# Optimization experiments

Measured on AMD Instinct MI355X. Metric: run time of the kernel, lower is better.

Reference implementation:

```python
import jax, jax.numpy as jnp
import numpy as np

# ---- single-qubit gate matrices (theta may be scalar or batched (N,)) ----

def _rx(theta):
    t = theta * 0.5
    c = jnp.cos(t).astype(jnp.complex64)
    s = jnp.sin(t).astype(jnp.complex64)
    return jnp.stack([jnp.stack([c, -1j * s], -1), jnp.stack([-1j * s, c], -1)], -2)

def _ry(theta):
    t = theta * 0.5
    c = jnp.cos(t).astype(jnp.complex64)
    s = jnp.sin(t).astype(jnp.complex64)
    return jnp.stack([jnp.stack([c, -s], -1), jnp.stack([s, c], -1)], -2)

def _rz(theta):
    t = theta * 0.5
    e = jnp.exp(-1j * t.astype(jnp.complex64))
    z = jnp.zeros_like(e)
    return jnp.stack([jnp.stack([e, z], -1), jnp.stack([z, jnp.conj(e)], -1)], -2)

def _apply_1q(state, U, wire):
    # state: (N, 2^P) complex; U: (2,2) shared or (N,2,2) per-sample
    N = state.shape[0]
    s = state.reshape(N, 2 ** wire, 2, -1)
    if U.ndim == 3:
        s = jnp.einsum('nab,nxby->nxay', U, s)
    else:
        s = jnp.einsum('ab,nxby->nxay', U, s)
    return s.reshape(N, -1)

def _apply_cnot(state, c, t, P):
    # flip target axis where control bit == 1
    N = state.shape[0]
    s = state.reshape((N,) + (2,) * P)
    ac, at = 1 + c, 1 + t
    s0 = jnp.take(s, 0, axis=ac)
    s1 = jnp.take(s, 1, axis=ac)
    at2 = at if at < ac else at - 1
    s1 = jnp.flip(s1, axis=at2)
    s = jnp.stack([s0, s1], axis=ac)
    return s.reshape(N, -1)

def _circuit(angles, qweights, P):
    # angles: (N, P, 3); qweights: (L, P, 3) -> expvals (N, P)
    N = angles.shape[0]
    state = jnp.zeros((N, 2 ** P), jnp.complex64).at[:, 0].set(1.0)
    for i in range(P):  # encoding rotations (per-sample)
        state = _apply_1q(state, _rx(angles[:, i, 0]), i)
        state = _apply_1q(state, _ry(angles[:, i, 1]), i)
        state = _apply_1q(state, _rz(angles[:, i, 2]), i)
    for L in range(qweights.shape[0]):  # variational layers (shared weights)
        for i in range(P):
            state = _apply_1q(state, _ry(qweights[L, i, 0]), i)
            state = _apply_1q(state, _rz(qweights[L, i, 1]), i)
            state = _apply_1q(state, _ry(qweights[L, i, 2]), i)
        for i in range(P):  # ring CNOTs
            state = _apply_cnot(state, i, (i + 1) % P, P)
    probs = jnp.real(state * jnp.conj(state))  # (N, 2^P)
    idx = jnp.arange(2 ** P)
    bits = (idx[None, :] >> (P - 1 - jnp.arange(P))[:, None]) & 1  # wire 0 = MSB
    signs = (1 - 2 * bits).astype(jnp.float32)  # (P, 2^P)
    return probs @ signs.T  # <Z_i> per wire, (N, P)

def setup_inputs() -> dict:
    key = jax.random.key(0)
    ks = jax.random.split(key, 6)
    B, T, P, D, L = 2, 128, 13, 64, 2
    h = jax.random.normal(ks[0], (B, T, P, D), jnp.float32)
    enc_w = jax.random.normal(ks[1], (3, D), jnp.float32) * (1.0 / np.sqrt(D))
    enc_b = jax.random.normal(ks[2], (3,), jnp.float32) * 0.1
    qweights = jax.random.normal(ks[3], (L, P, 3), jnp.float32)
    dec_w = jax.random.normal(ks[4], (D, 1), jnp.float32) * 0.1
    alpha = jnp.full((1,), 0.05, jnp.float32)
    return {"h": h, "enc_w": enc_w, "enc_b": enc_b, "qweights": qweights, "dec_w": dec_w, "alpha": alpha}

def reference(h, enc_w, enc_b, qweights, dec_w, alpha):
    B, T, P, D = h.shape
    # encoder: Linear(D, 3)
    angles = (jnp.einsum('btpd,ad->btpa', h, enc_w) + enc_b).reshape(B * T, P, 3)
    expvals = _circuit(angles, qweights, P)  # (B*T, P)
    # decoder: Linear(1, D, bias=False)
    decoded = (expvals[:, :, None] * dec_w[:, 0][None, None, :]).reshape(B, T, P, D)
    return h + alpha[0] * decoded
```

## Files before the change

kernel.cpp:

```cpp
#include <hip/hip_runtime.h>

#define P   13
#define BLK 512
#define NH  (P * 64)

typedef float2 c2;

__device__ __forceinline__ c2 cmul2(c2 a, c2 b) {
    return make_float2(a.x * b.x - a.y * b.y, a.x * b.y + a.y * b.x);
}
__device__ __forceinline__ c2 cfma2(c2 a, c2 b, c2 c) {
    return make_float2(fmaf(a.x, b.x, fmaf(-a.y, b.y, c.x)),
                       fmaf(a.x, b.y, fmaf( a.y, b.x, c.y)));
}
__device__ __forceinline__ c2 shflx2(c2 v, int m) {
    c2 r;
    r.x = __shfl_xor(v.x, m, 64);
    r.y = __shfl_xor(v.y, m, 64);
    return r;
}


__global__ __launch_bounds__(BLK) void qlc_kernel(
    const float* __restrict__ h, const float* __restrict__ enc_w,
    const float* __restrict__ enc_b, const float* __restrict__ qw,
    const float* __restrict__ dec_w, const float* __restrict__ alpha,
    float* __restrict__ out, int nlayers)
{
    const int n    = blockIdx.x;
    const int tid  = threadIdx.x;
    const int lane = tid & 63;
    const int wv   = tid >> 6;

    __shared__ float lds[16384];
    float* re = lds;
    float* im = lds + 8192;

    c2 s[16];

    for (int p = wv; p < P; p += 8) {
        float hv = h[(size_t)n * NH + p * 64 + lane];
        float a0 = hv * enc_w[lane];
        float a1 = hv * enc_w[64 + lane];
        float a2 = hv * enc_w[128 + lane];
#pragma unroll
        for (int m = 32; m; m >>= 1) {
            a0 += __shfl_xor(a0, m, 64);
            a1 += __shfl_xor(a1, m, 64);
            a2 += __shfl_xor(a2, m, 64);
        }
        float x = 0.5f * (a0 + enc_b[0]);
        float y = 0.5f * (a1 + enc_b[1]);
        float z = 0.5f * (a2 + enc_b[2]);
        float cx = cosf(x), sx = sinf(x);
        float cy = cosf(y), sy = sinf(y);
        float cz = cosf(z), sz = sinf(z);
        c2 em = {cz, -sz}, ep = {cz, sz};
        c2 u0 = cmul2(em, make_float2(cy * cx,  sy * sx));
        c2 u1 = cmul2(ep, make_float2(sy * cx, -cy * sx));
        c2 w0 = u0, w1 = u1;
        if (nlayers > 0) {
            const float* w = qw + p * 3;
            float a = 0.5f * w[0], b = 0.5f * w[1], c = 0.5f * w[2];
            float ca = cosf(a), sa = sinf(a);
            float cb = cosf(b), sb = sinf(b);
            float cc = cosf(c), sc = sinf(c);
            c2 B00 = { ca * cb, -ca * sb};
            c2 B01 = {-sa * cb,  sa * sb};
            c2 B10 = { sa * cb,  sa * sb};
            c2 B11 = { ca * cb,  ca * sb};
            c2 V00 = {cc * B00.x - sc * B10.x, cc * B00.y - sc * B10.y};
            c2 V01 = {cc * B01.x - sc * B11.x, cc * B01.y - sc * B11.y};
            c2 V10 = {sc * B00.x + cc * B10.x, sc * B00.y + cc * B10.y};
            c2 V11 = {sc * B01.x + cc * B11.x, sc * B01.y + cc * B11.y};
            w0 = cfma2(V00, u0, cmul2(V01, u1));
            w1 = cfma2(V10, u0, cmul2(V11, u1));
        }
        if (lane == 0) {
            lds[p * 4 + 0] = w0.x; lds[p * 4 + 1] = w0.y;
            lds[p * 4 + 2] = w1.x; lds[p * 4 + 3] = w1.y;
        }
    }
    __syncthreads();
    {
        c2 pref = {1.f, 0.f};
#pragma unroll
        for (int w = 0; w < 9; ++w) {
            int b = (tid >> (8 - w)) & 1;
            c2 vp = {lds[w * 4 + b * 2], lds[w * 4 + b * 2 + 1]};
            pref = cmul2(pref, vp);
        }
        c2 w9[2], w10[2], w11[2], w12[2];
#pragma unroll
        for (int b = 0; b < 2; ++b) {
            w9[b]  = {lds[ 9 * 4 + b * 2], lds[ 9 * 4 + b * 2 + 1]};
            w10[b] = {lds[10 * 4 + b * 2], lds[10 * 4 + b * 2 + 1]};
            w11[b] = {lds[11 * 4 + b * 2], lds[11 * 4 + b * 2 + 1]};
            w12[b] = {lds[12 * 4 + b * 2], lds[12 * 4 + b * 2 + 1]};
        }
#pragma unroll
        for (int r = 0; r < 16; ++r)
            s[r] = cmul2(pref, cmul2(cmul2(w9[(r >> 3) & 1], w10[(r >> 2) & 1]),
                                     cmul2(w11[(r >> 1) & 1], w12[r & 1])));
    }

    auto cnot_chain = [&]() {
        __syncthreads();
        {
            int c = (tid >> 8) & 1;
            if (c) {
#pragma unroll
                for (int r = 0; r < 16; ++r) { re[r * 512 + tid] = s[r].x; im[r * 512 + tid] = s[r].y; }
            }
            __syncthreads();
            if (c) {
                int p = tid ^ 128;
#pragma unroll
                for (int r = 0; r < 16; ++r) s[r] = make_float2(re[r * 512 + p], im[r * 512 + p]);
            }
        }
        __syncthreads();
        {
            int c = (tid >> 7) & 1;
            if (c) {
#pragma unroll
                for (int r = 0; r < 16; ++r) { re[r * 512 + tid] = s[r].x; im[r * 512 + tid] = s[r].y; }
            }
            __syncthreads();
            if (c) {
                int p = tid ^ 64;
#pragma unroll
                for (int r = 0; r < 16; ++r) s[r] = make_float2(re[r * 512 + p], im[r * 512 + p]);
            }
        }
        {
            int c = (tid >> 6) & 1;
#pragma unroll
            for (int r = 0; r < 16; ++r) { c2 pv = shflx2(s[r], 32); if (c) s[r] = pv; }
        }
#pragma unroll
        for (int k = 0; k < 5; ++k) {
            int cb = 5 - k, m = 1 << (4 - k);
            int c = (lane >> cb) & 1;
#pragma unroll
            for (int r = 0; r < 16; ++r) { c2 pv = shflx2(s[r], m); if (c) s[r] = pv; }
        }
        {
            int c = lane & 1;
#pragma unroll
            for (int r = 0; r < 8; ++r) {
                c2 a = s[r], b = s[r + 8];
                s[r]     = c ? b : a;
                s[r + 8] = c ? a : b;
            }
        }
#pragma unroll
        for (int r = 0; r < 16; ++r)
            if ((r & 8) && !(r & 4)) { c2 t = s[r]; s[r] = s[r | 4]; s[r | 4] = t; }
#pragma unroll
        for (int r = 0; r < 16; ++r)
            if ((r & 4) && !(r & 2)) { c2 t = s[r]; s[r] = s[r | 2]; s[r | 2] = t; }
#pragma unroll
        for (int r = 0; r < 16; ++r)
            if ((r & 2) && !(r & 1)) { c2 t = s[r]; s[r] = s[r | 1]; s[r | 1] = t; }
        __syncthreads();
#pragma unroll
        for (int r = 1; r < 16; r += 2) { re[r * 512 + tid] = s[r].x; im[r * 512 + tid] = s[r].y; }
        __syncthreads();
        {
            int p = tid ^ 256;
#pragma unroll
            for (int r = 1; r < 16; r += 2) s[r] = make_float2(re[r * 512 + p], im[r * 512 + p]);
        }
    };

    auto apply_layer = [&](int l) {
        __syncthreads();
        if (tid < P) {
            const float* w = qw + (size_t)(l * P + tid) * 3;
            float a = 0.5f * w[0], b = 0.5f * w[1], c = 0.5f * w[2];
            float ca = cosf(a), sa = sinf(a);
            float cb = cosf(b), sb = sinf(b);
            float cc = cosf(c), sc = sinf(c);
            c2 B00 = { ca * cb, -ca * sb};
            c2 B01 = {-sa * cb,  sa * sb};
            c2 B10 = { sa * cb,  sa * sb};
            c2 B11 = { ca * cb,  ca * sb};
            float* m = lds + tid * 8;
            m[0] = cc * B00.x - sc * B10.x; m[1] = cc * B00.y - sc * B10.y;
            m[2] = cc * B01.x - sc * B11.x; m[3] = cc * B01.y - sc * B11.y;
            m[4] = sc * B00.x + cc * B10.x; m[5] = sc * B00.y + cc * B10.y;
            m[6] = sc * B01.x + cc * B11.x; m[7] = sc * B01.y + cc * B11.y;
        }
        __syncthreads();
#pragma unroll
        for (int p = 9; p <= 12; ++p) {
            int b = 12 - p;
            c2 u00 = {lds[p * 8 + 0], lds[p * 8 + 1]}, u01 = {lds[p * 8 + 2], lds[p * 8 + 3]};
            c2 u10 = {lds[p * 8 + 4], lds[p * 8 + 5]}, u11 = {lds[p * 8 + 6], lds[p * 8 + 7]};
#pragma unroll
            for (int r = 0; r < 16; ++r)
                if (!(r & (1 << b))) {
                    int r1 = r | (1 << b);
                    c2 a0 = s[r], a1 = s[r1];
                    s[r]  = cfma2(u00, a0, cmul2(u01, a1));
                    s[r1] = cfma2(u10, a0, cmul2(u11, a1));
                }
        }
#pragma unroll
        for (int p = 3; p <= 8; ++p) {
            int lb = 8 - p;
            c2 u00 = {lds[p * 8 + 0], lds[p * 8 + 1]}, u01 = {lds[p * 8 + 2], lds[p * 8 + 3]};
            c2 u10 = {lds[p * 8 + 4], lds[p * 8 + 5]}, u11 = {lds[p * 8 + 6], lds[p * 8 + 7]};
            int mb = (lane >> lb) & 1;
            c2 ua = mb ? u11 : u00;
            c2 ub = mb ? u10 : u01;
#pragma unroll
            for (int r = 0; r < 16; ++r) {
                c2 pv = shflx2(s[r], 1 << lb);
                s[r] = cfma2(ua, s[r], cmul2(ub, pv));
            }
        }
        c2 um[3][4];
#pragma unroll
        for (int p = 0; p < 3; ++p) {
            um[p][0] = {lds[p * 8 + 0], lds[p * 8 + 1]};
            um[p][1] = {lds[p * 8 + 2], lds[p * 8 + 3]};
            um[p][2] = {lds[p * 8 + 4], lds[p * 8 + 5]};
            um[p][3] = {lds[p * 8 + 6], lds[p * 8 + 7]};
        }
#pragma unroll
        for (int p = 0; p < 3; ++p) {
            int shift = 8 - p;
            __syncthreads();
#pragma unroll
            for (int r = 0; r < 16; ++r) { re[r * 512 + tid] = s[r].x; im[r * 512 + tid] = s[r].y; }
            __syncthreads();
            int pt = tid ^ (1 << shift);
            int mb = (tid >> shift) & 1;
            c2 ua = mb ? um[p][3] : um[p][0];
            c2 ub = mb ? um[p][2] : um[p][1];
#pragma unroll
            for (int r = 0; r < 16; ++r) {
                c2 pv = make_float2(re[r * 512 + pt], im[r * 512 + pt]);
                s[r] = cfma2(ua, s[r], cmul2(ub, pv));
            }
        }
    };

    if (nlayers > 0) cnot_chain();
    for (int l = 1; l < nlayers; ++l) { apply_layer(l); cnot_chain(); }

    float tot = 0.f, e9 = 0.f, e10 = 0.f, e11 = 0.f, e12 = 0.f;
#pragma unroll
    for (int r = 0; r < 16; ++r) {
        float pr = fmaf(s[r].x, s[r].x, s[r].y * s[r].y);
        tot += pr;
        e9  += (r & 8) ? -pr : pr;
        e10 += (r & 4) ? -pr : pr;
        e11 += (r & 2) ? -pr : pr;
        e12 += (r & 1) ? -pr : pr;
    }
    float v[13];
#pragma unroll
    for (int w = 0; w < 9; ++w) v[w] = ((tid >> (8 - w)) & 1) ? -tot : tot;
    v[9] = e9; v[10] = e10; v[11] = e11; v[12] = e12;
#pragma unroll
    for (int w = 0; w < 13; ++w) {
#pragma unroll
        for (int m = 32; m; m >>= 1) v[w] += __shfl_xor(v[w], m, 64);
    }
    __syncthreads();
    if (lane == 0) {
#pragma unroll
        for (int w = 0; w < 13; ++w) lds[wv * 13 + w] = v[w];
    }
    __syncthreads();
    if (tid < 13) {
        float sum = 0.f;
        for (int q = 0; q < 8; ++q) sum += lds[q * 13 + tid];
        lds[256 + tid] = sum;
    }
    __syncthreads();
    float al = alpha[0];
    for (int idx = tid; idx < NH; idx += BLK) {
        size_t off = (size_t)n * NH + idx;
        out[off] = fmaf(al * lds[256 + (idx >> 6)], dec_w[idx & 63], h[off]);
    }
}

extern "C" void kernel_launch(void* const* d_in, const int* in_sizes, int n_in,
                              void* d_out, int out_size, void* d_ws, size_t ws_size,
                              hipStream_t stream) {
    const float* h     = (const float*)d_in[0];
    const float* enc_w = (const float*)d_in[1];
    const float* enc_b = (const float*)d_in[2];
    const float* qw    = (const float*)d_in[3];
    const float* dec_w = (const float*)d_in[4];
    const float* alpha = (const float*)d_in[5];
    float* out = (float*)d_out;

    int N = in_sizes[0] / NH;
    int L = in_sizes[3] / (P * 3);

    qlc_kernel<<<N, BLK, 0, stream>>>(h, enc_w, enc_b, qw, dec_w, alpha, out, L);
}
```

Baseline: 91.11 us.

## Absorb CNOT rings into GF(2) basis-frame tracking instead of physically permuting state

Replaces the explicit CNOT-ring permutations (LDS round-trips and shuffles) with compile-time and runtime tracking of a linear GF(2) change of basis. The initial product state is built directly in the permuted frame, layer gates are applied along the transformed bit masks, and the Z expectations are read through parity masks. A specialised path for two layers uses constexpr masks so the gates map onto plain register, lane-shuffle and three LDS exchanges. It also switches to __sincosf and stores the state in LDS as interleaved float2. This removes several barrier-heavy shared-memory exchanges per layer, but the logic is intricate and __sincosf is less accurate than sinf/cosf.

```diff
diff --git a/kernel.cpp b/kernel.cpp
--- a/kernel.cpp
+++ b/kernel.cpp
@@ -14,12 +14,64 @@
                        fmaf(a.x, b.y, fmaf( a.y, b.x, c.y)));
 }
 __device__ __forceinline__ c2 shflx2(c2 v, int m) {
-    c2 r;
-    r.x = __shfl_xor(v.x, m, 64);
-    r.y = __shfl_xor(v.y, m, 64);
-    return r;
-}
-
+    c2 r; r.x = __shfl_xor(v.x, m, 64); r.y = __shfl_xor(v.y, m, 64); return r;
+}
+
+struct RowSet { unsigned r[13]; };
+constexpr RowSet chain_rows(RowSet f) {
+    for (int i = 0; i < 13; ++i) { int bc = 12 - i; int bt = (i == 12) ? 12 : (11 - i); f.r[bt] ^= f.r[bc]; }
+    return f;
+}
+constexpr RowSet chain_cols(RowSet g) {
+    for (int i = 0; i < 13; ++i) { int bc = 12 - i; int bt = (i == 12) ? 12 : (11 - i); g.r[bc] ^= g.r[bt]; }
+    return g;
+}
+constexpr RowSet R0c {{0x0C00,0x0801,0x0003,0x0006,0x000C,0x0018,0x0030,0x0060,0x00C0,0x0180,0x0300,0x1600,0x1400}};
+constexpr RowSet G0c {{0x1400,0x1C00,0x1C01,0x1C03,0x1C07,0x1C0F,0x1C1F,0x1C3F,0x1C7F,0x1CFF,0x1DFF,0x1FFF,0x0FFF}};
+constexpr RowSet F1c = chain_rows(R0c);
+constexpr RowSet F2c = chain_rows(F1c);
+constexpr RowSet G1c = chain_cols(G0c);
+static_assert(G1c.r[0]==0x0400 && G1c.r[1]==0x0800 && G1c.r[2]==0x0001 && G1c.r[3]==0x0002 &&
+              G1c.r[4]==0x0004 && G1c.r[5]==0x0008 && G1c.r[6]==0x0010 && G1c.r[7]==0x0020 &&
+              G1c.r[8]==0x0040 && G1c.r[9]==0x0080 && G1c.r[10]==0x0100 && G1c.r[11]==0x0200 &&
+              G1c.r[12]==0x1000, "single-bit gate masks after chain 1");
+static_assert(F1c.r[0]==0x0400 && F1c.r[1]==0x0800 && F1c.r[2]==0x0001 && F1c.r[12]==0x1000,
+              "frame after chain 1 is the bit-permutation phi");
+
+__device__ __forceinline__ void build_V(float wa, float wb, float wc, c2* u) {
+    float a = 0.5f * wa, b = 0.5f * wb, c = 0.5f * wc;
+    float sa, ca, sb, cb, sc, cc;
+    __sincosf(a, &sa, &ca); __sincosf(b, &sb, &cb); __sincosf(c, &sc, &cc);
+    float A = ca * cb, Bq = ca * sb, C = sa * cb, D = sa * sb;
+    u[0] = make_float2( cc * A - sc * C, -cc * Bq - sc * D);
+    u[1] = make_float2(-cc * C - sc * A,  cc * D - sc * Bq);
+    u[2] = make_float2( sc * A + cc * C, -sc * Bq + cc * D);
+    u[3] = make_float2(-sc * C + cc * A,  sc * D + cc * Bq);
+}
+
+template<int K>
+__device__ __forceinline__ void gate_reg(c2* s, const float* m) {
+    c2 u00 = {m[0], m[1]}, u01 = {m[2], m[3]}, u10 = {m[4], m[5]}, u11 = {m[6], m[7]};
+#pragma unroll
+    for (int r = 0; r < 16; ++r)
+        if (!(r & (1 << K))) {
+            const int r1 = r | (1 << K);
+            c2 a0 = s[r], a1 = s[r1];
+            s[r]  = cfma2(u00, a0, cmul2(u01, a1));
+            s[r1] = cfma2(u10, a0, cmul2(u11, a1));
+        }
+}
+template<int LM>
+__device__ __forceinline__ void gate_lane(c2* s, const float* m, int lane) {
+    c2 u00 = {m[0], m[1]}, u01 = {m[2], m[3]}, u10 = {m[4], m[5]}, u11 = {m[6], m[7]};
+    int mb = (lane & LM) ? 1 : 0;
+    c2 ua = mb ? u11 : u00, ub = mb ? u10 : u01;
+#pragma unroll
+    for (int r = 0; r < 16; ++r) {
+        c2 pv = shflx2(s[r], LM);
+        s[r] = cfma2(ua, s[r], cmul2(ub, pv));
+    }
+}
 
 __global__ __launch_bounds__(BLK) void qlc_kernel(
     const float* __restrict__ h, const float* __restrict__ enc_w,
@@ -27,265 +79,193 @@
     const float* __restrict__ dec_w, const float* __restrict__ alpha,
     float* __restrict__ out, int nlayers)
 {
-    const int n    = blockIdx.x;
-    const int tid  = threadIdx.x;
-    const int lane = tid & 63;
-    const int wv   = tid >> 6;
-
-    __shared__ float lds[16384];
-    float* re = lds;
-    float* im = lds + 8192;
-
+    const int n = blockIdx.x, tid = threadIdx.x, lane = tid & 63, wv = tid >> 6;
+    __shared__ c2 plane[8192];
+    float* smem = (float*)plane;
+    float* vec  = smem;
+    float* mats = smem + 64;
     c2 s[16];
 
     for (int p = wv; p < P; p += 8) {
         float hv = h[(size_t)n * NH + p * 64 + lane];
-        float a0 = hv * enc_w[lane];
-        float a1 = hv * enc_w[64 + lane];
-        float a2 = hv * enc_w[128 + lane];
+        float a0 = hv * enc_w[lane], a1 = hv * enc_w[64 + lane], a2 = hv * enc_w[128 + lane];
 #pragma unroll
         for (int m = 32; m; m >>= 1) {
-            a0 += __shfl_xor(a0, m, 64);
-            a1 += __shfl_xor(a1, m, 64);
-            a2 += __shfl_xor(a2, m, 64);
-        }
-        float x = 0.5f * (a0 + enc_b[0]);
-        float y = 0.5f * (a1 + enc_b[1]);
-        float z = 0.5f * (a2 + enc_b[2]);
-        float cx = cosf(x), sx = sinf(x);
-        float cy = cosf(y), sy = sinf(y);
-        float cz = cosf(z), sz = sinf(z);
+            a0 += __shfl_xor(a0, m, 64); a1 += __shfl_xor(a1, m, 64); a2 += __shfl_xor(a2, m, 64);
+        }
+        float x = 0.5f * (a0 + enc_b[0]), y = 0.5f * (a1 + enc_b[1]), z = 0.5f * (a2 + enc_b[2]);
+        float sx, cx, sy, cy, sz, cz;
+        __sincosf(x, &sx, &cx); __sincosf(y, &sy, &cy); __sincosf(z, &sz, &cz);
         c2 em = {cz, -sz}, ep = {cz, sz};
         c2 u0 = cmul2(em, make_float2(cy * cx,  sy * sx));
         c2 u1 = cmul2(ep, make_float2(sy * cx, -cy * sx));
         c2 w0 = u0, w1 = u1;
         if (nlayers > 0) {
-            const float* w = qw + p * 3;
-            float a = 0.5f * w[0], b = 0.5f * w[1], c = 0.5f * w[2];
-            float ca = cosf(a), sa = sinf(a);
-            float cb = cosf(b), sb = sinf(b);
-            float cc = cosf(c), sc = sinf(c);
-            c2 B00 = { ca * cb, -ca * sb};
-            c2 B01 = {-sa * cb,  sa * sb};
-            c2 B10 = { sa * cb,  sa * sb};
-            c2 B11 = { ca * cb,  ca * sb};
-            c2 V00 = {cc * B00.x - sc * B10.x, cc * B00.y - sc * B10.y};
-            c2 V01 = {cc * B01.x - sc * B11.x, cc * B01.y - sc * B11.y};
-            c2 V10 = {sc * B00.x + cc * B10.x, sc * B00.y + cc * B10.y};
-            c2 V11 = {sc * B01.x + cc * B11.x, sc * B01.y + cc * B11.y};
-            w0 = cfma2(V00, u0, cmul2(V01, u1));
-            w1 = cfma2(V10, u0, cmul2(V11, u1));
+            c2 u[4]; const float* q = qw + p * 3;
+            build_V(q[0], q[1], q[2], u);
+            w0 = cfma2(u[0], u0, cmul2(u[1], u1));
+            w1 = cfma2(u[2], u0, cmul2(u[3], u1));
         }
         if (lane == 0) {
-            lds[p * 4 + 0] = w0.x; lds[p * 4 + 1] = w0.y;
-            lds[p * 4 + 2] = w1.x; lds[p * 4 + 3] = w1.y;
-        }
-    }
-    __syncthreads();
+            int b = 12 - p;
+            vec[b*4+0] = w0.x; vec[b*4+1] = w0.y; vec[b*4+2] = w1.x; vec[b*4+3] = w1.y;
+        }
+    }
+    if (nlayers == 2 && wv == 5 && lane < P) {
+        c2 u[4]; const float* q = qw + (P + lane) * 3;
+        build_V(q[0], q[1], q[2], u);
+        float* m = mats + lane * 8;
+        m[0]=u[0].x; m[1]=u[0].y; m[2]=u[1].x; m[3]=u[1].y;
+        m[4]=u[2].x; m[5]=u[2].y; m[6]=u[3].x; m[7]=u[3].y;
+    }
+    __syncthreads();
+
     {
         c2 pref = {1.f, 0.f};
-#pragma unroll
-        for (int w = 0; w < 9; ++w) {
-            int b = (tid >> (8 - w)) & 1;
-            c2 vp = {lds[w * 4 + b * 2], lds[w * 4 + b * 2 + 1]};
-            pref = cmul2(pref, vp);
-        }
-        c2 w9[2], w10[2], w11[2], w12[2];
-#pragma unroll
-        for (int b = 0; b < 2; ++b) {
-            w9[b]  = {lds[ 9 * 4 + b * 2], lds[ 9 * 4 + b * 2 + 1]};
-            w10[b] = {lds[10 * 4 + b * 2], lds[10 * 4 + b * 2 + 1]};
-            w11[b] = {lds[11 * 4 + b * 2], lds[11 * 4 + b * 2 + 1]};
-            w12[b] = {lds[12 * 4 + b * 2], lds[12 * 4 + b * 2 + 1]};
-        }
-#pragma unroll
-        for (int r = 0; r < 16; ++r)
-            s[r] = cmul2(pref, cmul2(cmul2(w9[(r >> 3) & 1], w10[(r >> 2) & 1]),
-                                     cmul2(w11[(r >> 1) & 1], w12[r & 1])));
-    }
-
-    auto cnot_chain = [&]() {
+        const int UB[8] = {0, 6, 7, 8, 9, 10, 11, 12};
+#pragma unroll
+        for (int k = 0; k < 8; ++k) {
+            const int b = UB[k];
+            int t = __popc(tid & (R0c.r[b] >> 4)) & 1;
+            c2 vv = { vec[b*4 + t*2], vec[b*4 + t*2 + 1] };
+            pref = cmul2(pref, vv);
+        }
+        int t1 = (tid >> 7) & 1, t5 = tid & 1;
+        c2 w1v[2] = { {vec[4+t1*2], vec[5+t1*2]}, {vec[4+(t1^1)*2], vec[5+(t1^1)*2]} };
+        c2 w2v[2] = { {vec[8],  vec[9]},  {vec[10], vec[11]} };
+        c2 w3v[2] = { {vec[12], vec[13]}, {vec[14], vec[15]} };
+        c2 w4v[2] = { {vec[16], vec[17]}, {vec[18], vec[19]} };
+        c2 w5v[2] = { {vec[20+t5*2], vec[21+t5*2]}, {vec[20+(t5^1)*2], vec[21+(t5^1)*2]} };
+        c2 v12[4], v34[4], P5[2];
+        v12[0]=cmul2(w1v[0],w2v[0]); v12[1]=cmul2(w1v[0],w2v[1]);
+        v12[2]=cmul2(w1v[1],w2v[0]); v12[3]=cmul2(w1v[1],w2v[1]);
+        v34[0]=cmul2(w3v[0],w4v[0]); v34[1]=cmul2(w3v[0],w4v[1]);
+        v34[2]=cmul2(w3v[1],w4v[0]); v34[3]=cmul2(w3v[1],w4v[1]);
+        P5[0]=cmul2(pref,w5v[0]); P5[1]=cmul2(pref,w5v[1]);
+#pragma unroll
+        for (int r = 0; r < 16; ++r) {
+            const int i12 = ((r & 1) << 1) | ((r ^ (r >> 1)) & 1);
+            const int i34 = ((((r >> 1) ^ (r >> 2)) & 1) << 1) | (((r >> 2) ^ (r >> 3)) & 1);
+            s[r] = cmul2(P5[(r >> 3) & 1], cmul2(v12[i12], v34[i34]));
+        }
+    }
+
+    unsigned mrows[13];
+
+    if (nlayers == 2) {
+        gate_reg<0>(s, mats + 10*8);
+        gate_reg<1>(s, mats +  9*8);
+        gate_reg<2>(s, mats +  8*8);
+        gate_reg<3>(s, mats +  7*8);
+        gate_lane<1 >(s, mats + 6*8, lane);
+        gate_lane<2 >(s, mats + 5*8, lane);
+        gate_lane<4 >(s, mats + 4*8, lane);
+        gate_lane<8 >(s, mats + 3*8, lane);
+        gate_lane<16>(s, mats + 2*8, lane);
+        gate_lane<32>(s, mats + 1*8, lane);
+        c2 umA[4], umB[4], umC[4];
+#pragma unroll
+        for (int j = 0; j < 4; ++j) {
+            umA[j] = { mats[12*8 + j*2], mats[12*8 + j*2 + 1] };
+            umB[j] = { mats[11*8 + j*2], mats[11*8 + j*2 + 1] };
+            umC[j] = { mats[ 0*8 + j*2], mats[ 0*8 + j*2 + 1] };
+        }
         __syncthreads();
         {
-            int c = (tid >> 8) & 1;
-            if (c) {
-#pragma unroll
-                for (int r = 0; r < 16; ++r) { re[r * 512 + tid] = s[r].x; im[r * 512 + tid] = s[r].y; }
+            const c2* um[3] = {umA, umB, umC};
+            const int  tx[3] = {64, 128, 256};
+#pragma unroll
+            for (int g = 0; g < 3; ++g) {
+#pragma unroll
+                for (int r = 0; r < 16; ++r) plane[r*512 + tid] = s[r];
+                __syncthreads();
+                int pt = tid ^ tx[g];
+                int mb = (tid & tx[g]) ? 1 : 0;
+                c2 ua = mb ? um[g][3] : um[g][0];
+                c2 ub = mb ? um[g][2] : um[g][1];
+#pragma unroll
+                for (int r = 0; r < 16; ++r) {
+                    c2 pv = plane[r*512 + pt];
+                    s[r] = cfma2(ua, s[r], cmul2(ub, pv));
+                }
+                __syncthreads();
             }
-            __syncthreads();
-            if (c) {
-                int p = tid ^ 128;
-#pragma unroll
-                for (int r = 0; r < 16; ++r) s[r] = make_float2(re[r * 512 + p], im[r * 512 + p]);
+        }
+#pragma unroll
+        for (int b = 0; b < 13; ++b) mrows[b] = F2c.r[b];
+    } else {
+        unsigned rowF[13], colG[13];
+#pragma unroll
+        for (int b = 0; b < 13; ++b) { rowF[b] = R0c.r[b]; colG[b] = G0c.r[b]; }
+        for (int l = 1; l < nlayers; ++l) {
+#pragma unroll
+            for (int i = 0; i < P; ++i) { int bc = 12-i, bt = (i==12)?12:(11-i); rowF[bt]^=rowF[bc]; colG[bc]^=colG[bt]; }
+#pragma unroll
+            for (int b = 0; b < 13; ++b) {
+                const float* q = qw + ((size_t)l * P + (12 - b)) * 3;
+                c2 u[4]; build_V(q[0], q[1], q[2], u);
+                __syncthreads();
+#pragma unroll
+                for (int r = 0; r < 16; ++r) plane[r*512 + tid] = s[r];
+                __syncthreads();
+                unsigned m = colG[b], row = rowF[b];
+                int pt = tid ^ (int)(m >> 4);
+                unsigned mr = m & 15, rl = row & 15;
+                int bt_ = __popc(tid & (row >> 4)) & 1;
+#pragma unroll
+                for (int r = 0; r < 16; ++r) {
+                    c2 pv = plane[((r ^ mr) & 15) * 512 + pt];
+                    int beta = bt_ ^ (__popc(r & rl) & 1);
+                    c2 ua = beta ? u[3] : u[0], ub = beta ? u[2] : u[1];
+                    s[r] = cfma2(ua, s[r], cmul2(ub, pv));
+                }
             }
         }
-        __syncthreads();
-        {
-            int c = (tid >> 7) & 1;
-            if (c) {
-#pragma unroll
-                for (int r = 0; r < 16; ++r) { re[r * 512 + tid] = s[r].x; im[r * 512 + tid] = s[r].y; }
-            }
-            __syncthreads();
-            if (c) {
-                int p = tid ^ 64;
-#pragma unroll
-                for (int r = 0; r < 16; ++r) s[r] = make_float2(re[r * 512 + p], im[r * 512 + p]);
-            }
-        }
-        {
-            int c = (tid >> 6) & 1;
-#pragma unroll
-            for (int r = 0; r < 16; ++r) { c2 pv = shflx2(s[r], 32); if (c) s[r] = pv; }
-        }
-#pragma unroll
-        for (int k = 0; k < 5; ++k) {
-            int cb = 5 - k, m = 1 << (4 - k);
-            int c = (lane >> cb) & 1;
-#pragma unroll
-            for (int r = 0; r < 16; ++r) { c2 pv = shflx2(s[r], m); if (c) s[r] = pv; }
-        }
-        {
-            int c = lane & 1;
-#pragma unroll
-            for (int r = 0; r < 8; ++r) {
-                c2 a = s[r], b = s[r + 8];
-                s[r]     = c ? b : a;
-                s[r + 8] = c ? a : b;
-            }
-        }
+        if (nlayers >= 1) {
+#pragma unroll
+            for (int i = 0; i < P; ++i) { int bc = 12-i, bt = (i==12)?12:(11-i); rowF[bt]^=rowF[bc]; colG[bc]^=colG[bt]; }
+        }
+#pragma unroll
+        for (int b = 0; b < 13; ++b) mrows[b] = rowF[b];
+    }
+
+    float pr[16];
+#pragma unroll
+    for (int r = 0; r < 16; ++r) pr[r] = fmaf(s[r].x, s[r].x, s[r].y * s[r].y);
+    float ev[13];
+#pragma unroll
+    for (int b = 0; b < 13; ++b) {
+        unsigned row = mrows[b];
+        int tp = __popc(tid & (row >> 4)) & 1;
+        float acc = 0.f;
 #pragma unroll
         for (int r = 0; r < 16; ++r)
-            if ((r & 8) && !(r & 4)) { c2 t = s[r]; s[r] = s[r | 4]; s[r | 4] = t; }
-#pragma unroll
-        for (int r = 0; r < 16; ++r)
-            if ((r & 4) && !(r & 2)) { c2 t = s[r]; s[r] = s[r | 2]; s[r | 2] = t; }
-#pragma unroll
-        for (int r = 0; r < 16; ++r)
-            if ((r & 2) && !(r & 1)) { c2 t = s[r]; s[r] = s[r | 1]; s[r | 1] = t; }
-        __syncthreads();
-#pragma unroll
-        for (int r = 1; r < 16; r += 2) { re[r * 512 + tid] = s[r].x; im[r * 512 + tid] = s[r].y; }
-        __syncthreads();
-        {
-            int p = tid ^ 256;
-#pragma unroll
-            for (int r = 1; r < 16; r += 2) s[r] = make_float2(re[r * 512 + p], im[r * 512 + p]);
-        }
-    };
-
-    auto apply_layer = [&](int l) {
-        __syncthreads();
-        if (tid < P) {
-            const float* w = qw + (size_t)(l * P + tid) * 3;
-            float a = 0.5f * w[0], b = 0.5f * w[1], c = 0.5f * w[2];
-            float ca = cosf(a), sa = sinf(a);
-            float cb = cosf(b), sb = sinf(b);
-            float cc = cosf(c), sc = sinf(c);
-            c2 B00 = { ca * cb, -ca * sb};
-            c2 B01 = {-sa * cb,  sa * sb};
-            c2 B10 = { sa * cb,  sa * sb};
-            c2 B11 = { ca * cb,  ca * sb};
-            float* m = lds + tid * 8;
-            m[0] = cc * B00.x - sc * B10.x; m[1] = cc * B00.y - sc * B10.y;
-            m[2] = cc * B01.x - sc * B11.x; m[3] = cc * B01.y - sc * B11.y;
-            m[4] = sc * B00.x + cc * B10.x; m[5] = sc * B00.y + cc * B10.y;
-            m[6] = sc * B01.x + cc * B11.x; m[7] = sc * B01.y + cc * B11.y;
-        }
-        __syncthreads();
-#pragma unroll
-        for (int p = 9; p <= 12; ++p) {
-            int b = 12 - p;
-            c2 u00 = {lds[p * 8 + 0], lds[p * 8 + 1]}, u01 = {lds[p * 8 + 2], lds[p * 8 + 3]};
-            c2 u10 = {lds[p * 8 + 4], lds[p * 8 + 5]}, u11 = {lds[p * 8 + 6], lds[p * 8 + 7]};
-#pragma unroll
-            for (int r = 0; r < 16; ++r)
-                if (!(r & (1 << b))) {
-                    int r1 = r | (1 << b);
-                    c2 a0 = s[r], a1 = s[r1];
-                    s[r]  = cfma2(u00, a0, cmul2(u01, a1));
-                    s[r1] = cfma2(u10, a0, cmul2(u11, a1));
-                }
-        }
-#pragma unroll
-        for (int p = 3; p <= 8; ++p) {
-            int lb = 8 - p;
-            c2 u00 = {lds[p * 8 + 0], lds[p * 8 + 1]}, u01 = {lds[p * 8 + 2], lds[p * 8 + 3]};
-            c2 u10 = {lds[p * 8 + 4], lds[p * 8 + 5]}, u11 = {lds[p * 8 + 6], lds[p * 8 + 7]};
-            int mb = (lane >> lb) & 1;
-            c2 ua = mb ? u11 : u00;
-            c2 ub = mb ? u10 : u01;
-#pragma unroll
-            for (int r = 0; r < 16; ++r) {
-                c2 pv = shflx2(s[r], 1 << lb);
-                s[r] = cfma2(ua, s[r], cmul2(ub, pv));
-            }
-        }
-        c2 um[3][4];
-#pragma unroll
-        for (int p = 0; p < 3; ++p) {
-            um[p][0] = {lds[p * 8 + 0], lds[p * 8 + 1]};
-            um[p][1] = {lds[p * 8 + 2], lds[p * 8 + 3]};
-            um[p][2] = {lds[p * 8 + 4], lds[p * 8 + 5]};
-            um[p][3] = {lds[p * 8 + 6], lds[p * 8 + 7]};
-        }
-#pragma unroll
-        for (int p = 0; p < 3; ++p) {
-            int shift = 8 - p;
-            __syncthreads();
-#pragma unroll
-            for (int r = 0; r < 16; ++r) { re[r * 512 + tid] = s[r].x; im[r * 512 + tid] = s[r].y; }
-            __syncthreads();
-            int pt = tid ^ (1 << shift);
-            int mb = (tid >> shift) & 1;
-            c2 ua = mb ? um[p][3] : um[p][0];
-            c2 ub = mb ? um[p][2] : um[p][1];
-#pragma unroll
-            for (int r = 0; r < 16; ++r) {
-                c2 pv = make_float2(re[r * 512 + pt], im[r * 512 + pt]);
-                s[r] = cfma2(ua, s[r], cmul2(ub, pv));
-            }
-        }
-    };
-
-    if (nlayers > 0) cnot_chain();
-    for (int l = 1; l < nlayers; ++l) { apply_layer(l); cnot_chain(); }
-
-    float tot = 0.f, e9 = 0.f, e10 = 0.f, e11 = 0.f, e12 = 0.f;
-#pragma unroll
-    for (int r = 0; r < 16; ++r) {
-        float pr = fmaf(s[r].x, s[r].x, s[r].y * s[r].y);
-        tot += pr;
-        e9  += (r & 8) ? -pr : pr;
-        e10 += (r & 4) ? -pr : pr;
-        e11 += (r & 2) ? -pr : pr;
-        e12 += (r & 1) ? -pr : pr;
-    }
-    float v[13];
-#pragma unroll
-    for (int w = 0; w < 9; ++w) v[w] = ((tid >> (8 - w)) & 1) ? -tot : tot;
-    v[9] = e9; v[10] = e10; v[11] = e11; v[12] = e12;
+            acc += (__popc((unsigned)r & row) & 1) ? -pr[r] : pr[r];
+        ev[12 - b] = tp ? -acc : acc;
+    }
 #pragma unroll
     for (int w = 0; w < 13; ++w) {
 #pragma unroll
-        for (int m = 32; m; m >>= 1) v[w] += __shfl_xor(v[w], m, 64);
-    }
+        for (int m = 32; m; m >>= 1) ev[w] += __shfl_xor(ev[w], m, 64);
+    }
+    float* red  = smem + 256;
+    float* red2 = smem + 384;
     __syncthreads();
     if (lane == 0) {
 #pragma unroll
-        for (int w = 0; w < 13; ++w) lds[wv * 13 + w] = v[w];
+        for (int w = 0; w < 13; ++w) red[wv * 13 + w] = ev[w];
     }
     __syncthreads();
     if (tid < 13) {
         float sum = 0.f;
-        for (int q = 0; q < 8; ++q) sum += lds[q * 13 + tid];
-        lds[256 + tid] = sum;
+        for (int q = 0; q < 8; ++q) sum += red[q * 13 + tid];
+        red2[tid] = sum;
     }
     __syncthreads();
     float al = alpha[0];
     for (int idx = tid; idx < NH; idx += BLK) {
         size_t off = (size_t)n * NH + idx;
-        out[off] = fmaf(al * lds[256 + (idx >> 6)], dec_w[idx & 63], h[off]);
+        out[off] = fmaf(al * red2[idx >> 6], dec_w[idx & 63], h[off]);
     }
 }
 
```

Result: faster. 81.16 us (-10.9%).
